# Kernel optimization log

Measured on AMD Instinct MI355X. Metric: run time of the kernel, lower is better.

## Reference

```python
import jax, jax.numpy as jnp
import numpy as np

B, S, D, H = 2, 2048, 1024, 16
RANK = int(D * 0.2)  # 204, per decom(): rank = int(min(a,b)*ratio_LR)
HEAD = D // H


def setup_inputs() -> dict:
    key = jax.random.key(0)
    ks = jax.random.split(key, 16)
    s_in = 1.0 / np.sqrt(D)
    s_r = 1.0 / np.sqrt(RANK)
    inp = {
        'q': jax.random.normal(ks[0], (B, S, D), jnp.float32),
        'k': jax.random.normal(ks[1], (B, S, D), jnp.float32),
        'v': jax.random.normal(ks[2], (B, S, D), jnp.float32),
    }
    names = ['q', 'k', 'v', 'o']
    for i, n in enumerate(names):
        inp[f'V{n}'] = jax.random.uniform(ks[3 + 3 * i], (RANK, D), jnp.float32, -s_in, s_in)
        inp[f'U{n}'] = jax.random.uniform(ks[4 + 3 * i], (D, RANK), jnp.float32, -s_r, s_r)
        inp[f'b{n}'] = jax.random.uniform(ks[5 + 3 * i], (D,), jnp.float32, -s_r, s_r)
    return inp


def _factorized(x, Vw, Uw, b):
    # x @ V^T @ U^T + b  (low-rank linear: Linear(D->rank, no bias) then Linear(rank->D, bias))
    return jnp.einsum('bsr,dr->bsd', jnp.einsum('bsd,rd->bsr', x, Vw), Uw) + b


def _split_heads(x):
    # [B,S,D] -> [B,H,S,HEAD]
    return x.reshape(B, S, H, HEAD).transpose(0, 2, 1, 3)


def reference(q, k, v, Vq, Uq, bq, Vk, Uk, bk, Vv, Uv, bv, Vo, Uo, bo):
    qh = _split_heads(_factorized(q, Vq, Uq, bq))
    kh = _split_heads(_factorized(k, Vk, Uk, bk))
    vh = _split_heads(_factorized(v, Vv, Uv, bv))
    temperature = jnp.asarray(HEAD, jnp.float32) ** 0.5
    scores = jnp.einsum('bhqd,bhkd->bhqk', qh, kh) / temperature
    causal = jnp.tril(jnp.ones((S, S), bool))  # recreated each call in original
    scores = jnp.where(causal, scores, -jnp.inf)
    attn = jax.nn.softmax(scores, axis=-1)  # [B,H,S,S]
    out = jnp.einsum('bhqk,bhkd->bhqd', attn, vh)
    out = out.transpose(0, 2, 1, 3).reshape(B, S, D)
    out = _factorized(out, Vo, Uo, bo)
    # original returns attn flattened over batch*heads
    return out, attn.reshape(B * H, S, S)
```

## Files before the change

### kernel.cpp

```cpp
#include <hip/hip_runtime.h>
#include <stdint.h>

#define BB   2
#define SS   2048
#define DD   1024
#define NH   16
#define RK   204
#define RKP  256
#define HDIM 64
#define BH   (BB*NH)

typedef __attribute__((ext_vector_type(8))) short short8;
typedef __attribute__((ext_vector_type(4))) float f32x4;
typedef unsigned short u16;
typedef unsigned int   u32;

#define NEGBIG (-1e30f)

static __device__ __forceinline__ u16 f2bf(float f) {
    union { float f; u32 u; } v; v.f = f;
    u32 u = v.u;
    return (u16)((u + 0x7fffu + ((u >> 16) & 1u)) >> 16);
}
static __device__ __forceinline__ u32 pack2(float lo, float hi) {
    return (u32)f2bf(lo) | ((u32)f2bf(hi) << 16);
}

__global__ void cvt_bf16_k(const float* __restrict__ in, u16* __restrict__ out, int n4) {
    int i = blockIdx.x * blockDim.x + threadIdx.x;
    if (i < n4) {
        float4 f = ((const float4*)in)[i];
        u32 lo = pack2(f.x, f.y), hi = pack2(f.z, f.w);
        ((uint2*)out)[i] = make_uint2(lo, hi);
    }
}

__global__ void cvt_pad_u_k(const float* __restrict__ in, u16* __restrict__ out) {
    int i = blockIdx.x * blockDim.x + threadIdx.x;
    if (i >= DD * RKP) return;
    int row = i >> 8, col = i & (RKP - 1);
    out[i] = (col < RK) ? f2bf(in[row * RK + col]) : (u16)0;
}

__global__ __launch_bounds__(256)
void transpose_v_k(const u16* __restrict__ vh, u16* __restrict__ vT) {
    __shared__ __align__(16) u16 T[64*72];
    const int blk = blockIdx.x;
    const int st = blk & 31, bh = blk >> 5;
    const int b_ = bh >> 4, h = bh & (NH - 1);
    const int t = threadIdx.x;
    const int r = t >> 2, seg = t & 3;

    const u16* src = vh + (size_t)(b_*SS + st*64 + r)*DD + h*HDIM + seg*16;
    __align__(16) u16 vs_[16];
    *(uint4*)(vs_ + 0) = ((const uint4*)src)[0];
    *(uint4*)(vs_ + 8) = ((const uint4*)src)[1];
    #pragma unroll
    for (int j = 0; j < 16; ++j) T[(seg*16 + j)*72 + r] = vs_[j];
    __syncthreads();

    u16* dst = vT + ((size_t)bh*HDIM + r)*SS + st*64 + seg*16;
    ((uint4*)dst)[0] = *(const uint4*)(T + r*72 + seg*16);
    ((uint4*)dst)[1] = *(const uint4*)(T + r*72 + seg*16 + 8);
}

template<int A_F32, int OUT_F32, int HAS_BIAS>
__global__ __launch_bounds__(256)
void gemm_nt_k(const void* __restrict__ Ap, int lda,
               const u16* __restrict__ Bp, int ldb, int nrowsB,
               const float* __restrict__ bias,
               void* __restrict__ Cp, int ldc, int K)
{
    __shared__ __align__(16) u16 As[64*72];
    __shared__ __align__(16) u16 Bs[64*72];
    const int row0 = blockIdx.x * 64;
    const int col0 = blockIdx.y * 64;
    const int t = threadIdx.x;
    const int w = t >> 6, lane = t & 63, quad = lane >> 4, l16 = lane & 15;
    const int r = t >> 2, seg = t & 3;

    f32x4 acc0 = 0.f, acc1 = 0.f, acc2 = 0.f, acc3 = 0.f;

    for (int k0 = 0; k0 < K; k0 += 64) {
        __syncthreads();
        if (A_F32) {
            const float* ga = (const float*)Ap + (size_t)(row0 + r) * lda + k0 + seg*16;
            float4 f0 = ((const float4*)ga)[0];
            float4 f1 = ((const float4*)ga)[1];
            float4 f2 = ((const float4*)ga)[2];
            float4 f3 = ((const float4*)ga)[3];
            uint4 s0 = { pack2(f0.x,f0.y), pack2(f0.z,f0.w), pack2(f1.x,f1.y), pack2(f1.z,f1.w) };
            uint4 s1 = { pack2(f2.x,f2.y), pack2(f2.z,f2.w), pack2(f3.x,f3.y), pack2(f3.z,f3.w) };
            *(uint4*)(As + r*72 + seg*16)     = s0;
            *(uint4*)(As + r*72 + seg*16 + 8) = s1;
        } else {
            const u16* ga = (const u16*)Ap + (size_t)(row0 + r) * lda + k0 + seg*16;
            *(uint4*)(As + r*72 + seg*16)     = ((const uint4*)ga)[0];
            *(uint4*)(As + r*72 + seg*16 + 8) = ((const uint4*)ga)[1];
        }
        {
            uint4 b0 = {0,0,0,0}, b1 = {0,0,0,0};
            if (col0 + r < nrowsB) {
                const u16* gb = Bp + (size_t)(col0 + r) * ldb + k0 + seg*16;
                b0 = ((const uint4*)gb)[0];
                b1 = ((const uint4*)gb)[1];
            }
            *(uint4*)(Bs + r*72 + seg*16)     = b0;
            *(uint4*)(Bs + r*72 + seg*16 + 8) = b1;
        }
        __syncthreads();
        #pragma unroll
        for (int c = 0; c < 2; ++c) {
            short8 a = *(const short8*)(As + (w*16 + l16)*72 + c*32 + quad*8);
            short8 b0v = *(const short8*)(Bs + (0*16 + l16)*72 + c*32 + quad*8);
            acc0 = __builtin_amdgcn_mfma_f32_16x16x32_bf16(a, b0v, acc0, 0, 0, 0);
            short8 b1v = *(const short8*)(Bs + (1*16 + l16)*72 + c*32 + quad*8);
            acc1 = __builtin_amdgcn_mfma_f32_16x16x32_bf16(a, b1v, acc1, 0, 0, 0);
            short8 b2v = *(const short8*)(Bs + (2*16 + l16)*72 + c*32 + quad*8);
            acc2 = __builtin_amdgcn_mfma_f32_16x16x32_bf16(a, b2v, acc2, 0, 0, 0);
            short8 b3v = *(const short8*)(Bs + (3*16 + l16)*72 + c*32 + quad*8);
            acc3 = __builtin_amdgcn_mfma_f32_16x16x32_bf16(a, b3v, acc3, 0, 0, 0);
        }
    }

    #pragma unroll
    for (int f = 0; f < 4; ++f) {
        f32x4 a = (f==0) ? acc0 : (f==1) ? acc1 : (f==2) ? acc2 : acc3;
        int col = col0 + f*16 + l16;
        float bv = HAS_BIAS ? bias[col] : 0.f;
        #pragma unroll
        for (int rg = 0; rg < 4; ++rg) {
            int rowg = row0 + w*16 + quad*4 + rg;
            float val = a[rg] + bv;
            if (col >= nrowsB) val = 0.f;
            if (OUT_F32) ((float*)Cp)[(size_t)rowg*ldc + col] = val;
            else         ((u16*)Cp)[(size_t)rowg*ldc + col]  = f2bf(val);
        }
    }
}

__global__ __launch_bounds__(256)
void attn_ml_k(const u16* __restrict__ qh, const u16* __restrict__ kh,
               float* __restrict__ mbuf, float* __restrict__ lbuf)
{
    __shared__ __align__(16) u16 Ks[64*72];
    const int blk = blockIdx.x;
    const int qt = blk & 31, bh = blk >> 5;
    const int b_ = bh >> 4, h = bh & (NH - 1);
    const int qbase = qt * 64;
    const int t = threadIdx.x, w = t >> 6, lane = t & 63, quad = lane >> 4, l16 = lane & 15;
    const int r = t >> 2, seg = t & 3;
    const float scl = 0.125f;

    const u16* qrow = qh + (size_t)(b_*SS + qbase + w*16 + l16)*DD + h*HDIM;
    short8 q0 = *(const short8*)(qrow + quad*8);
    short8 q1 = *(const short8*)(qrow + 32 + quad*8);

    float m[4], l[4];
    #pragma unroll
    for (int rg = 0; rg < 4; ++rg) { m[rg] = NEGBIG; l[rg] = 0.f; }

    for (int kt = 0; kt <= qt; ++kt) {
        int kbase = kt * 64;
        __syncthreads();
        const u16* krow = kh + (size_t)(b_*SS + kbase + r)*DD + h*HDIM + seg*16;
        uint4 kv0 = ((const uint4*)krow)[0];
        uint4 kv1 = ((const uint4*)krow)[1];
        *(uint4*)(Ks + r*72 + seg*16)     = kv0;
        *(uint4*)(Ks + r*72 + seg*16 + 8) = kv1;
        __syncthreads();

        f32x4 sa0 = 0.f, sa1 = 0.f, sa2 = 0.f, sa3 = 0.f;
        {
            short8 b0 = *(const short8*)(Ks + (0*16 + l16)*72 + quad*8);
            sa0 = __builtin_amdgcn_mfma_f32_16x16x32_bf16(q0, b0, sa0, 0,0,0);
            short8 b0b = *(const short8*)(Ks + (0*16 + l16)*72 + 32 + quad*8);
            sa0 = __builtin_amdgcn_mfma_f32_16x16x32_bf16(q1, b0b, sa0, 0,0,0);
            short8 b1 = *(const short8*)(Ks + (1*16 + l16)*72 + quad*8);
            sa1 = __builtin_amdgcn_mfma_f32_16x16x32_bf16(q0, b1, sa1, 0,0,0);
            short8 b1b = *(const short8*)(Ks + (1*16 + l16)*72 + 32 + quad*8);
            sa1 = __builtin_amdgcn_mfma_f32_16x16x32_bf16(q1, b1b, sa1, 0,0,0);
            short8 b2 = *(const short8*)(Ks + (2*16 + l16)*72 + quad*8);
            sa2 = __builtin_amdgcn_mfma_f32_16x16x32_bf16(q0, b2, sa2, 0,0,0);
            short8 b2b = *(const short8*)(Ks + (2*16 + l16)*72 + 32 + quad*8);
            sa2 = __builtin_amdgcn_mfma_f32_16x16x32_bf16(q1, b2b, sa2, 0,0,0);
            short8 b3 = *(const short8*)(Ks + (3*16 + l16)*72 + quad*8);
            sa3 = __builtin_amdgcn_mfma_f32_16x16x32_bf16(q0, b3, sa3, 0,0,0);
            short8 b3b = *(const short8*)(Ks + (3*16 + l16)*72 + 32 + quad*8);
            sa3 = __builtin_amdgcn_mfma_f32_16x16x32_bf16(q1, b3b, sa3, 0,0,0);
        }

        if (kt < qt) {
            #pragma unroll
            for (int rg = 0; rg < 4; ++rg) {
                float v0 = sa0[rg]*scl, v1 = sa1[rg]*scl, v2 = sa2[rg]*scl, v3 = sa3[rg]*scl;
                float m4 = fmaxf(fmaxf(v0, v1), fmaxf(v2, v3));
                float nm = fmaxf(m[rg], m4);
                l[rg] = l[rg]*__expf(m[rg]-nm)
                      + (__expf(v0-nm)+__expf(v1-nm)) + (__expf(v2-nm)+__expf(v3-nm));
                m[rg] = nm;
            }
        } else {
            int key0 = kbase + l16;
            #pragma unroll
            for (int rg = 0; rg < 4; ++rg) {
                int qg = qbase + w*16 + quad*4 + rg;
                bool c0 = (key0      <= qg), c1 = (key0 + 16 <= qg);
                bool c2 = (key0 + 32 <= qg), c3 = (key0 + 48 <= qg);
                float v0 = c0 ? sa0[rg]*scl : NEGBIG;
                float v1 = c1 ? sa1[rg]*scl : NEGBIG;
                float v2 = c2 ? sa2[rg]*scl : NEGBIG;
                float v3 = c3 ? sa3[rg]*scl : NEGBIG;
                float m4 = fmaxf(fmaxf(v0, v1), fmaxf(v2, v3));
                float nm = fmaxf(m[rg], m4);
                float e0 = c0 ? __expf(v0-nm) : 0.f;
                float e1 = c1 ? __expf(v1-nm) : 0.f;
                float e2 = c2 ? __expf(v2-nm) : 0.f;
                float e3 = c3 ? __expf(v3-nm) : 0.f;
                float corr = (m[rg] > NEGBIG) ? __expf(m[rg]-nm) : 0.f;
                l[rg] = l[rg]*corr + (e0+e1) + (e2+e3);
                m[rg] = nm;
            }
        }
    }

    #pragma unroll
    for (int rg = 0; rg < 4; ++rg) {
        #pragma unroll
        for (int d = 1; d < 16; d <<= 1) {
            float mo = __shfl_xor(m[rg], d);
            float lo = __shfl_xor(l[rg], d);
            float nm = fmaxf(m[rg], mo);
            l[rg] = l[rg]*__expf(m[rg]-nm) + lo*__expf(mo-nm);
            m[rg] = nm;
        }
    }
    if (l16 == 0) {
        #pragma unroll
        for (int rg = 0; rg < 4; ++rg) {
            int qg = qbase + w*16 + quad*4 + rg;
            mbuf[bh*SS + qg] = m[rg];
            lbuf[bh*SS + qg] = l[rg];
        }
    }
}

__global__ __launch_bounds__(256)
void attn_av_k(const u16* __restrict__ qh, const u16* __restrict__ kh,
               const u16* __restrict__ vT,
               const float* __restrict__ mbuf, const float* __restrict__ lbuf,
               float* __restrict__ attn_out, u16* __restrict__ Ob)
{
    __shared__ __align__(16) u16 Ks[64*72];
    __shared__ __align__(16) u16 Vs[64*72];
    __shared__ __align__(16) u16 Ps[64*72];
    const int blk = blockIdx.x;
    const int qt = blk & 31, bh = blk >> 5;
    const int b_ = bh >> 4, h = bh & (NH - 1);
    const int qbase = qt * 64;
    const int t = threadIdx.x, w = t >> 6, lane = t & 63, quad = lane >> 4, l16 = lane & 15;
    const int r = t >> 2, seg = t & 3;
    const float scl = 0.125f;

    const u16* qrow = qh + (size_t)(b_*SS + qbase + w*16 + l16)*DD + h*HDIM;
    short8 q0 = *(const short8*)(qrow + quad*8);
    short8 q1 = *(const short8*)(qrow + 32 + quad*8);

    float mr[4], rl[4];
    #pragma unroll
    for (int rg = 0; rg < 4; ++rg) {
        int qg = qbase + w*16 + quad*4 + rg;
        mr[rg] = mbuf[bh*SS + qg];
        rl[rg] = 1.f / lbuf[bh*SS + qg];
    }
    f32x4 oa0 = 0.f, oa1 = 0.f, oa2 = 0.f, oa3 = 0.f;
    float* attn_base = attn_out + (size_t)bh * SS * SS;

    for (int kt = 0; kt <= qt; ++kt) {
        int kbase = kt * 64;
        __syncthreads();
        {
            const u16* krow = kh + (size_t)(b_*SS + kbase + r)*DD + h*HDIM + seg*16;
            *(uint4*)(Ks + r*72 + seg*16)     = ((const uint4*)krow)[0];
            *(uint4*)(Ks + r*72 + seg*16 + 8) = ((const uint4*)krow)[1];
            const u16* vrow = vT + ((size_t)(bh*HDIM + r))*SS + kbase + seg*16;
            *(uint4*)(Vs + r*72 + seg*16)     = ((const uint4*)vrow)[0];
            *(uint4*)(Vs + r*72 + seg*16 + 8) = ((const uint4*)vrow)[1];
        }
        __syncthreads();

        f32x4 sa0 = 0.f, sa1 = 0.f, sa2 = 0.f, sa3 = 0.f;
        {
            short8 b0 = *(const short8*)(Ks + (0*16 + l16)*72 + quad*8);
            sa0 = __builtin_amdgcn_mfma_f32_16x16x32_bf16(q0, b0, sa0, 0,0,0);
            short8 b0b = *(const short8*)(Ks + (0*16 + l16)*72 + 32 + quad*8);
            sa0 = __builtin_amdgcn_mfma_f32_16x16x32_bf16(q1, b0b, sa0, 0,0,0);
            short8 b1 = *(const short8*)(Ks + (1*16 + l16)*72 + quad*8);
            sa1 = __builtin_amdgcn_mfma_f32_16x16x32_bf16(q0, b1, sa1, 0,0,0);
            short8 b1b = *(const short8*)(Ks + (1*16 + l16)*72 + 32 + quad*8);
            sa1 = __builtin_amdgcn_mfma_f32_16x16x32_bf16(q1, b1b, sa1, 0,0,0);
            short8 b2 = *(const short8*)(Ks + (2*16 + l16)*72 + quad*8);
            sa2 = __builtin_amdgcn_mfma_f32_16x16x32_bf16(q0, b2, sa2, 0,0,0);
            short8 b2b = *(const short8*)(Ks + (2*16 + l16)*72 + 32 + quad*8);
            sa2 = __builtin_amdgcn_mfma_f32_16x16x32_bf16(q1, b2b, sa2, 0,0,0);
            short8 b3 = *(const short8*)(Ks + (3*16 + l16)*72 + quad*8);
            sa3 = __builtin_amdgcn_mfma_f32_16x16x32_bf16(q0, b3, sa3, 0,0,0);
            short8 b3b = *(const short8*)(Ks + (3*16 + l16)*72 + 32 + quad*8);
            sa3 = __builtin_amdgcn_mfma_f32_16x16x32_bf16(q1, b3b, sa3, 0,0,0);
        }

        if (kt < qt) {
            #pragma unroll
            for (int f = 0; f < 4; ++f) {
                f32x4 sv = (f==0) ? sa0 : (f==1) ? sa1 : (f==2) ? sa2 : sa3;
                int key = kbase + f*16 + l16;
                #pragma unroll
                for (int rg = 0; rg < 4; ++rg) {
                    int qg = qbase + w*16 + quad*4 + rg;
                    float p = __expf(sv[rg]*scl - mr[rg]) * rl[rg];
                    attn_base[(size_t)qg*SS + key] = p;
                    Ps[(w*16 + quad*4 + rg)*72 + f*16 + l16] = f2bf(p);
                }
            }
        } else {
            #pragma unroll
            for (int f = 0; f < 4; ++f) {
                f32x4 sv = (f==0) ? sa0 : (f==1) ? sa1 : (f==2) ? sa2 : sa3;
                int key = kbase + f*16 + l16;
                #pragma unroll
                for (int rg = 0; rg < 4; ++rg) {
                    int qg = qbase + w*16 + quad*4 + rg;
                    float p = (key <= qg) ? __expf(sv[rg]*scl - mr[rg]) * rl[rg] : 0.f;
                    attn_base[(size_t)qg*SS + key] = p;
                    Ps[(w*16 + quad*4 + rg)*72 + f*16 + l16] = f2bf(p);
                }
            }
        }
        asm volatile("" ::: "memory");

        #pragma unroll
        for (int c = 0; c < 2; ++c) {
            short8 pa = *(const short8*)(Ps + (w*16 + l16)*72 + c*32 + quad*8);
            short8 v0 = *(const short8*)(Vs + (0*16 + l16)*72 + c*32 + quad*8);
            oa0 = __builtin_amdgcn_mfma_f32_16x16x32_bf16(pa, v0, oa0, 0,0,0);
            short8 v1 = *(const short8*)(Vs + (1*16 + l16)*72 + c*32 + quad*8);
            oa1 = __builtin_amdgcn_mfma_f32_16x16x32_bf16(pa, v1, oa1, 0,0,0);
            short8 v2 = *(const short8*)(Vs + (2*16 + l16)*72 + c*32 + quad*8);
            oa2 = __builtin_amdgcn_mfma_f32_16x16x32_bf16(pa, v2, oa2, 0,0,0);
            short8 v3 = *(const short8*)(Vs + (3*16 + l16)*72 + c*32 + quad*8);
            oa3 = __builtin_amdgcn_mfma_f32_16x16x32_bf16(pa, v3, oa3, 0,0,0);
        }
    }

    for (int kt = qt + 1; kt < 32; ++kt) {
        int kbase = kt * 64;
        float4 z = {0.f, 0.f, 0.f, 0.f};
        float* p = attn_base + (size_t)(qbase + r)*SS + kbase + seg*16;
        ((float4*)p)[0] = z; ((float4*)p)[1] = z; ((float4*)p)[2] = z; ((float4*)p)[3] = z;
    }

    #pragma unroll
    for (int f = 0; f < 4; ++f) {
        f32x4 ov = (f==0) ? oa0 : (f==1) ? oa1 : (f==2) ? oa2 : oa3;
        #pragma unroll
        for (int rg = 0; rg < 4; ++rg) {
            int qg = qbase + w*16 + quad*4 + rg;
            Ob[(size_t)(b_*SS + qg)*DD + h*HDIM + f*16 + l16] = f2bf(ov[rg]);
        }
    }
}

extern "C" void kernel_launch(void* const* d_in, const int* in_sizes, int n_in,
                              void* d_out, int out_size, void* d_ws, size_t ws_size,
                              hipStream_t stream)
{
    const float* xs[3] = { (const float*)d_in[0], (const float*)d_in[1], (const float*)d_in[2] };
    const float* Vw[4] = { (const float*)d_in[3], (const float*)d_in[6], (const float*)d_in[9],  (const float*)d_in[12] };
    const float* Uw[4] = { (const float*)d_in[4], (const float*)d_in[7], (const float*)d_in[10], (const float*)d_in[13] };
    const float* bw[4] = { (const float*)d_in[5], (const float*)d_in[8], (const float*)d_in[11], (const float*)d_in[14] };

    char* ws = (char*)d_ws;
    size_t off = 0;
    auto alloc = [&](size_t bytes) -> char* {
        char* p = ws + off;
        off += (bytes + 255) & ~(size_t)255;
        return p;
    };
    u16* wV[4]; for (int i = 0; i < 4; ++i) wV[i] = (u16*)alloc((size_t)RK*DD*2);
    u16* wU[4]; for (int i = 0; i < 4; ++i) wU[i] = (u16*)alloc((size_t)DD*RKP*2);
    u16* Tb  = (u16*)alloc((size_t)BB*SS*RKP*2);
    u16* hb[3]; for (int i = 0; i < 3; ++i) hb[i] = (u16*)alloc((size_t)BB*SS*DD*2);
    u16* vTb = (u16*)alloc((size_t)BB*SS*DD*2);
    float* mbuf = (float*)alloc((size_t)BH*SS*4);
    float* lbuf = (float*)alloc((size_t)BH*SS*4);
    u16* Ob  = (u16*)alloc((size_t)BB*SS*DD*2);
    (void)ws_size; (void)in_sizes; (void)n_in; (void)out_size;

    for (int i = 0; i < 4; ++i)
        cvt_bf16_k<<<(RK*DD/4 + 255)/256, 256, 0, stream>>>(Vw[i], wV[i], RK*DD/4);
    for (int i = 0; i < 4; ++i)
        cvt_pad_u_k<<<(DD*RKP + 255)/256, 256, 0, stream>>>(Uw[i], wU[i]);

    const int MROWS = BB*SS;
    for (int p = 0; p < 3; ++p) {
        gemm_nt_k<1,0,0><<<dim3(MROWS/64, RKP/64), 256, 0, stream>>>(
            xs[p], DD, wV[p], DD, RK, nullptr, Tb, RKP, DD);
        gemm_nt_k<0,0,1><<<dim3(MROWS/64, DD/64), 256, 0, stream>>>(
            Tb, RKP, wU[p], RKP, DD, bw[p], hb[p], DD, RKP);
    }
    transpose_v_k<<<BH*32, 256, 0, stream>>>(hb[2], vTb);

    float* attn_out = (float*)d_out + (size_t)BB*SS*DD;
    attn_ml_k<<<BH*32, 256, 0, stream>>>(hb[0], hb[1], mbuf, lbuf);
    attn_av_k<<<BH*32, 256, 0, stream>>>(hb[0], hb[1], vTb, mbuf, lbuf, attn_out, Ob);

    gemm_nt_k<0,0,0><<<dim3(MROWS/64, RKP/64), 256, 0, stream>>>(
        Ob, DD, wV[3], DD, RK, nullptr, Tb, RKP, DD);
    gemm_nt_k<0,1,1><<<dim3(MROWS/64, DD/64), 256, 0, stream>>>(
        Tb, RKP, wU[3], RKP, DD, bw[3], d_out, DD, RKP);
}
```

Baseline: 837.1 us.

## Fuse attention passes, V transpose into GEMM epilogue, nontemporal attn stores

Merges the two attention kernels (row max/sum pass and probability/AV pass) into one kernel that runs both passes back-to-back per query tile. This keeps m/l in registers instead of a global buffer round trip and saves a launch. The V projection GEMM now writes its output already transposed through shared memory, which removes the separate transpose kernel and one full intermediate buffer. Stores of the large fp32 attention matrix become nontemporal to cut cache pollution. The fused kernel holds more shared memory and registers per block, which may reduce occupancy.

```diff
diff --git a/kernel.cpp b/kernel.cpp
--- a/kernel.cpp
+++ b/kernel.cpp
@@ -42,29 +42,7 @@
     out[i] = (col < RK) ? f2bf(in[row * RK + col]) : (u16)0;
 }
 
-__global__ __launch_bounds__(256)
-void transpose_v_k(const u16* __restrict__ vh, u16* __restrict__ vT) {
-    __shared__ __align__(16) u16 T[64*72];
-    const int blk = blockIdx.x;
-    const int st = blk & 31, bh = blk >> 5;
-    const int b_ = bh >> 4, h = bh & (NH - 1);
-    const int t = threadIdx.x;
-    const int r = t >> 2, seg = t & 3;
-
-    const u16* src = vh + (size_t)(b_*SS + st*64 + r)*DD + h*HDIM + seg*16;
-    __align__(16) u16 vs_[16];
-    *(uint4*)(vs_ + 0) = ((const uint4*)src)[0];
-    *(uint4*)(vs_ + 8) = ((const uint4*)src)[1];
-    #pragma unroll
-    for (int j = 0; j < 16; ++j) T[(seg*16 + j)*72 + r] = vs_[j];
-    __syncthreads();
-
-    u16* dst = vT + ((size_t)bh*HDIM + r)*SS + st*64 + seg*16;
-    ((uint4*)dst)[0] = *(const uint4*)(T + r*72 + seg*16);
-    ((uint4*)dst)[1] = *(const uint4*)(T + r*72 + seg*16 + 8);
-}
-
-template<int A_F32, int OUT_F32, int HAS_BIAS>
+template<int A_F32, int OUT_F32, int HAS_BIAS, int OUT_VT>
 __global__ __launch_bounds__(256)
 void gemm_nt_k(const void* __restrict__ Ap, int lda,
                const u16* __restrict__ Bp, int ldb, int nrowsB,
@@ -123,6 +101,29 @@
         }
     }
 
+    if (OUT_VT) {
+        __syncthreads();
+        #pragma unroll
+        for (int f = 0; f < 4; ++f) {
+            f32x4 a = (f==0) ? acc0 : (f==1) ? acc1 : (f==2) ? acc2 : acc3;
+            int col = f*16 + l16;
+            float bv = HAS_BIAS ? bias[col0 + col] : 0.f;
+            #pragma unroll
+            for (int rg = 0; rg < 4; ++rg) {
+                int rowl = w*16 + quad*4 + rg;
+                As[col*72 + rowl] = f2bf(a[rg] + bv);
+            }
+        }
+        __syncthreads();
+        const int b_ = row0 >> 11;
+        const int s0 = row0 & (SS - 1);
+        const int h  = col0 >> 6;
+        u16* dst = (u16*)Cp + ((size_t)((b_*NH + h)*HDIM + r))*SS + s0 + seg*16;
+        ((uint4*)dst)[0] = *(const uint4*)(As + r*72 + seg*16);
+        ((uint4*)dst)[1] = *(const uint4*)(As + r*72 + seg*16 + 8);
+        return;
+    }
+
     #pragma unroll
     for (int f = 0; f < 4; ++f) {
         f32x4 a = (f==0) ? acc0 : (f==1) ? acc1 : (f==2) ? acc2 : acc3;
@@ -139,11 +140,33 @@
     }
 }
 
+#define QKT_8(sa0,sa1,sa2,sa3) do { \
+    short8 b0 = *(const short8*)(Ks + (0*16 + l16)*72 + quad*8); \
+    sa0 = __builtin_amdgcn_mfma_f32_16x16x32_bf16(q0, b0, sa0, 0,0,0); \
+    short8 b0b = *(const short8*)(Ks + (0*16 + l16)*72 + 32 + quad*8); \
+    sa0 = __builtin_amdgcn_mfma_f32_16x16x32_bf16(q1, b0b, sa0, 0,0,0); \
+    short8 b1 = *(const short8*)(Ks + (1*16 + l16)*72 + quad*8); \
+    sa1 = __builtin_amdgcn_mfma_f32_16x16x32_bf16(q0, b1, sa1, 0,0,0); \
+    short8 b1b = *(const short8*)(Ks + (1*16 + l16)*72 + 32 + quad*8); \
+    sa1 = __builtin_amdgcn_mfma_f32_16x16x32_bf16(q1, b1b, sa1, 0,0,0); \
+    short8 b2 = *(const short8*)(Ks + (2*16 + l16)*72 + quad*8); \
+    sa2 = __builtin_amdgcn_mfma_f32_16x16x32_bf16(q0, b2, sa2, 0,0,0); \
+    short8 b2b = *(const short8*)(Ks + (2*16 + l16)*72 + 32 + quad*8); \
+    sa2 = __builtin_amdgcn_mfma_f32_16x16x32_bf16(q1, b2b, sa2, 0,0,0); \
+    short8 b3 = *(const short8*)(Ks + (3*16 + l16)*72 + quad*8); \
+    sa3 = __builtin_amdgcn_mfma_f32_16x16x32_bf16(q0, b3, sa3, 0,0,0); \
+    short8 b3b = *(const short8*)(Ks + (3*16 + l16)*72 + 32 + quad*8); \
+    sa3 = __builtin_amdgcn_mfma_f32_16x16x32_bf16(q1, b3b, sa3, 0,0,0); \
+} while (0)
+
 __global__ __launch_bounds__(256)
-void attn_ml_k(const u16* __restrict__ qh, const u16* __restrict__ kh,
-               float* __restrict__ mbuf, float* __restrict__ lbuf)
+void attn_k(const u16* __restrict__ qh, const u16* __restrict__ kh,
+            const u16* __restrict__ vT,
+            float* __restrict__ attn_out, u16* __restrict__ Ob)
 {
     __shared__ __align__(16) u16 Ks[64*72];
+    __shared__ __align__(16) u16 Vs[64*72];
+    __shared__ __align__(16) u16 Ps[64*72];
     const int blk = blockIdx.x;
     const int qt = blk & 31, bh = blk >> 5;
     const int b_ = bh >> 4, h = bh & (NH - 1);
@@ -156,39 +179,24 @@
     short8 q0 = *(const short8*)(qrow + quad*8);
     short8 q1 = *(const short8*)(qrow + 32 + quad*8);
 
+    const u16* kstage = kh + (size_t)(b_*SS + r)*DD + h*HDIM + seg*16;
+    const u16* vstage = vT + ((size_t)(bh*HDIM + r))*SS + seg*16;
+
     float m[4], l[4];
     #pragma unroll
     for (int rg = 0; rg < 4; ++rg) { m[rg] = NEGBIG; l[rg] = 0.f; }
 
     for (int kt = 0; kt <= qt; ++kt) {
-        int kbase = kt * 64;
-        __syncthreads();
-        const u16* krow = kh + (size_t)(b_*SS + kbase + r)*DD + h*HDIM + seg*16;
-        uint4 kv0 = ((const uint4*)krow)[0];
-        uint4 kv1 = ((const uint4*)krow)[1];
-        *(uint4*)(Ks + r*72 + seg*16)     = kv0;
-        *(uint4*)(Ks + r*72 + seg*16 + 8) = kv1;
+        __syncthreads();
+        {
+            const u16* krow = kstage + (size_t)kt*64*DD;
+            *(uint4*)(Ks + r*72 + seg*16)     = ((const uint4*)krow)[0];
+            *(uint4*)(Ks + r*72 + seg*16 + 8) = ((const uint4*)krow)[1];
+        }
         __syncthreads();
 
         f32x4 sa0 = 0.f, sa1 = 0.f, sa2 = 0.f, sa3 = 0.f;
-        {
-            short8 b0 = *(const short8*)(Ks + (0*16 + l16)*72 + quad*8);
-            sa0 = __builtin_amdgcn_mfma_f32_16x16x32_bf16(q0, b0, sa0, 0,0,0);
-            short8 b0b = *(const short8*)(Ks + (0*16 + l16)*72 + 32 + quad*8);
-            sa0 = __builtin_amdgcn_mfma_f32_16x16x32_bf16(q1, b0b, sa0, 0,0,0);
-            short8 b1 = *(const short8*)(Ks + (1*16 + l16)*72 + quad*8);
-            sa1 = __builtin_amdgcn_mfma_f32_16x16x32_bf16(q0, b1, sa1, 0,0,0);
-            short8 b1b = *(const short8*)(Ks + (1*16 + l16)*72 + 32 + quad*8);
-            sa1 = __builtin_amdgcn_mfma_f32_16x16x32_bf16(q1, b1b, sa1, 0,0,0);
-            short8 b2 = *(const short8*)(Ks + (2*16 + l16)*72 + quad*8);
-            sa2 = __builtin_amdgcn_mfma_f32_16x16x32_bf16(q0, b2, sa2, 0,0,0);
-            short8 b2b = *(const short8*)(Ks + (2*16 + l16)*72 + 32 + quad*8);
-            sa2 = __builtin_amdgcn_mfma_f32_16x16x32_bf16(q1, b2b, sa2, 0,0,0);
-            short8 b3 = *(const short8*)(Ks + (3*16 + l16)*72 + quad*8);
-            sa3 = __builtin_amdgcn_mfma_f32_16x16x32_bf16(q0, b3, sa3, 0,0,0);
-            short8 b3b = *(const short8*)(Ks + (3*16 + l16)*72 + 32 + quad*8);
-            sa3 = __builtin_amdgcn_mfma_f32_16x16x32_bf16(q1, b3b, sa3, 0,0,0);
-        }
+        QKT_8(sa0, sa1, sa2, sa3);
 
         if (kt < qt) {
             #pragma unroll
@@ -201,7 +209,7 @@
                 m[rg] = nm;
             }
         } else {
-            int key0 = kbase + l16;
+            int key0 = kt*64 + l16;
             #pragma unroll
             for (int rg = 0; rg < 4; ++rg) {
                 int qg = qbase + w*16 + quad*4 + rg;
@@ -235,94 +243,51 @@
             m[rg] = nm;
         }
     }
-    if (l16 == 0) {
-        #pragma unroll
-        for (int rg = 0; rg < 4; ++rg) {
-            int qg = qbase + w*16 + quad*4 + rg;
-            mbuf[bh*SS + qg] = m[rg];
-            lbuf[bh*SS + qg] = l[rg];
-        }
-    }
-}
-
-__global__ __launch_bounds__(256)
-void attn_av_k(const u16* __restrict__ qh, const u16* __restrict__ kh,
-               const u16* __restrict__ vT,
-               const float* __restrict__ mbuf, const float* __restrict__ lbuf,
-               float* __restrict__ attn_out, u16* __restrict__ Ob)
-{
-    __shared__ __align__(16) u16 Ks[64*72];
-    __shared__ __align__(16) u16 Vs[64*72];
-    __shared__ __align__(16) u16 Ps[64*72];
-    const int blk = blockIdx.x;
-    const int qt = blk & 31, bh = blk >> 5;
-    const int b_ = bh >> 4, h = bh & (NH - 1);
-    const int qbase = qt * 64;
-    const int t = threadIdx.x, w = t >> 6, lane = t & 63, quad = lane >> 4, l16 = lane & 15;
-    const int r = t >> 2, seg = t & 3;
-    const float scl = 0.125f;
-
-    const u16* qrow = qh + (size_t)(b_*SS + qbase + w*16 + l16)*DD + h*HDIM;
-    short8 q0 = *(const short8*)(qrow + quad*8);
-    short8 q1 = *(const short8*)(qrow + 32 + quad*8);
-
     float mr[4], rl[4];
     #pragma unroll
-    for (int rg = 0; rg < 4; ++rg) {
-        int qg = qbase + w*16 + quad*4 + rg;
-        mr[rg] = mbuf[bh*SS + qg];
-        rl[rg] = 1.f / lbuf[bh*SS + qg];
-    }
+    for (int rg = 0; rg < 4; ++rg) { mr[rg] = m[rg]; rl[rg] = 1.f / l[rg]; }
+
     f32x4 oa0 = 0.f, oa1 = 0.f, oa2 = 0.f, oa3 = 0.f;
     float* attn_base = attn_out + (size_t)bh * SS * SS;
+    float* rp0 = attn_base + (size_t)(qbase + w*16 + quad*4 + 0)*SS + l16;
+    float* rp1 = attn_base + (size_t)(qbase + w*16 + quad*4 + 1)*SS + l16;
+    float* rp2 = attn_base + (size_t)(qbase + w*16 + quad*4 + 2)*SS + l16;
+    float* rp3 = attn_base + (size_t)(qbase + w*16 + quad*4 + 3)*SS + l16;
 
     for (int kt = 0; kt <= qt; ++kt) {
-        int kbase = kt * 64;
         __syncthreads();
         {
-            const u16* krow = kh + (size_t)(b_*SS + kbase + r)*DD + h*HDIM + seg*16;
+            const u16* krow = kstage + (size_t)kt*64*DD;
             *(uint4*)(Ks + r*72 + seg*16)     = ((const uint4*)krow)[0];
             *(uint4*)(Ks + r*72 + seg*16 + 8) = ((const uint4*)krow)[1];
-            const u16* vrow = vT + ((size_t)(bh*HDIM + r))*SS + kbase + seg*16;
+            const u16* vrow = vstage + kt*64;
             *(uint4*)(Vs + r*72 + seg*16)     = ((const uint4*)vrow)[0];
             *(uint4*)(Vs + r*72 + seg*16 + 8) = ((const uint4*)vrow)[1];
         }
         __syncthreads();
 
         f32x4 sa0 = 0.f, sa1 = 0.f, sa2 = 0.f, sa3 = 0.f;
-        {
-            short8 b0 = *(const short8*)(Ks + (0*16 + l16)*72 + quad*8);
-            sa0 = __builtin_amdgcn_mfma_f32_16x16x32_bf16(q0, b0, sa0, 0,0,0);
-            short8 b0b = *(const short8*)(Ks + (0*16 + l16)*72 + 32 + quad*8);
-            sa0 = __builtin_amdgcn_mfma_f32_16x16x32_bf16(q1, b0b, sa0, 0,0,0);
-            short8 b1 = *(const short8*)(Ks + (1*16 + l16)*72 + quad*8);
-            sa1 = __builtin_amdgcn_mfma_f32_16x16x32_bf16(q0, b1, sa1, 0,0,0);
-            short8 b1b = *(const short8*)(Ks + (1*16 + l16)*72 + 32 + quad*8);
-            sa1 = __builtin_amdgcn_mfma_f32_16x16x32_bf16(q1, b1b, sa1, 0,0,0);
-            short8 b2 = *(const short8*)(Ks + (2*16 + l16)*72 + quad*8);
-            sa2 = __builtin_amdgcn_mfma_f32_16x16x32_bf16(q0, b2, sa2, 0,0,0);
-            short8 b2b = *(const short8*)(Ks + (2*16 + l16)*72 + 32 + quad*8);
-            sa2 = __builtin_amdgcn_mfma_f32_16x16x32_bf16(q1, b2b, sa2, 0,0,0);
-            short8 b3 = *(const short8*)(Ks + (3*16 + l16)*72 + quad*8);
-            sa3 = __builtin_amdgcn_mfma_f32_16x16x32_bf16(q0, b3, sa3, 0,0,0);
-            short8 b3b = *(const short8*)(Ks + (3*16 + l16)*72 + 32 + quad*8);
-            sa3 = __builtin_amdgcn_mfma_f32_16x16x32_bf16(q1, b3b, sa3, 0,0,0);
-        }
+        QKT_8(sa0, sa1, sa2, sa3);
 
         if (kt < qt) {
             #pragma unroll
             for (int f = 0; f < 4; ++f) {
                 f32x4 sv = (f==0) ? sa0 : (f==1) ? sa1 : (f==2) ? sa2 : sa3;
-                int key = kbase + f*16 + l16;
-                #pragma unroll
-                for (int rg = 0; rg < 4; ++rg) {
-                    int qg = qbase + w*16 + quad*4 + rg;
-                    float p = __expf(sv[rg]*scl - mr[rg]) * rl[rg];
-                    attn_base[(size_t)qg*SS + key] = p;
-                    Ps[(w*16 + quad*4 + rg)*72 + f*16 + l16] = f2bf(p);
-                }
+                float p0 = __expf(sv[0]*scl - mr[0]) * rl[0];
+                float p1 = __expf(sv[1]*scl - mr[1]) * rl[1];
+                float p2 = __expf(sv[2]*scl - mr[2]) * rl[2];
+                float p3 = __expf(sv[3]*scl - mr[3]) * rl[3];
+                __builtin_nontemporal_store(p0, rp0 + f*16);
+                __builtin_nontemporal_store(p1, rp1 + f*16);
+                __builtin_nontemporal_store(p2, rp2 + f*16);
+                __builtin_nontemporal_store(p3, rp3 + f*16);
+                Ps[(w*16 + quad*4 + 0)*72 + f*16 + l16] = f2bf(p0);
+                Ps[(w*16 + quad*4 + 1)*72 + f*16 + l16] = f2bf(p1);
+                Ps[(w*16 + quad*4 + 2)*72 + f*16 + l16] = f2bf(p2);
+                Ps[(w*16 + quad*4 + 3)*72 + f*16 + l16] = f2bf(p3);
             }
         } else {
+            int kbase = kt*64;
             #pragma unroll
             for (int f = 0; f < 4; ++f) {
                 f32x4 sv = (f==0) ? sa0 : (f==1) ? sa1 : (f==2) ? sa2 : sa3;
@@ -331,11 +296,14 @@
                 for (int rg = 0; rg < 4; ++rg) {
                     int qg = qbase + w*16 + quad*4 + rg;
                     float p = (key <= qg) ? __expf(sv[rg]*scl - mr[rg]) * rl[rg] : 0.f;
-                    attn_base[(size_t)qg*SS + key] = p;
+                    float* rp = (rg==0) ? rp0 : (rg==1) ? rp1 : (rg==2) ? rp2 : rp3;
+                    __builtin_nontemporal_store(p, rp + f*16);
                     Ps[(w*16 + quad*4 + rg)*72 + f*16 + l16] = f2bf(p);
                 }
             }
         }
+        rp0 += 64; rp1 += 64; rp2 += 64; rp3 += 64;
+
         asm volatile("" ::: "memory");
 
         #pragma unroll
@@ -354,9 +322,12 @@
 
     for (int kt = qt + 1; kt < 32; ++kt) {
         int kbase = kt * 64;
-        float4 z = {0.f, 0.f, 0.f, 0.f};
+        f32x4 z = 0.f;
         float* p = attn_base + (size_t)(qbase + r)*SS + kbase + seg*16;
-        ((float4*)p)[0] = z; ((float4*)p)[1] = z; ((float4*)p)[2] = z; ((float4*)p)[3] = z;
+        __builtin_nontemporal_store(z, (f32x4*)p + 0);
+        __builtin_nontemporal_store(z, (f32x4*)p + 1);
+        __builtin_nontemporal_store(z, (f32x4*)p + 2);
+        __builtin_nontemporal_store(z, (f32x4*)p + 3);
     }
 
     #pragma unroll
@@ -389,10 +360,8 @@
     u16* wV[4]; for (int i = 0; i < 4; ++i) wV[i] = (u16*)alloc((size_t)RK*DD*2);
     u16* wU[4]; for (int i = 0; i < 4; ++i) wU[i] = (u16*)alloc((size_t)DD*RKP*2);
     u16* Tb  = (u16*)alloc((size_t)BB*SS*RKP*2);
-    u16* hb[3]; for (int i = 0; i < 3; ++i) hb[i] = (u16*)alloc((size_t)BB*SS*DD*2);
+    u16* hb[2]; for (int i = 0; i < 2; ++i) hb[i] = (u16*)alloc((size_t)BB*SS*DD*2);
     u16* vTb = (u16*)alloc((size_t)BB*SS*DD*2);
-    float* mbuf = (float*)alloc((size_t)BH*SS*4);
-    float* lbuf = (float*)alloc((size_t)BH*SS*4);
     u16* Ob  = (u16*)alloc((size_t)BB*SS*DD*2);
     (void)ws_size; (void)in_sizes; (void)n_in; (void)out_size;
 
@@ -402,20 +371,22 @@
         cvt_pad_u_k<<<(DD*RKP + 255)/256, 256, 0, stream>>>(Uw[i], wU[i]);
 
     const int MROWS = BB*SS;
-    for (int p = 0; p < 3; ++p) {
-        gemm_nt_k<1,0,0><<<dim3(MROWS/64, RKP/64), 256, 0, stream>>>(
+    for (int p = 0; p < 2; ++p) {
+        gemm_nt_k<1,0,0,0><<<dim3(MROWS/64, RKP/64), 256, 0, stream>>>(
             xs[p], DD, wV[p], DD, RK, nullptr, Tb, RKP, DD);
-        gemm_nt_k<0,0,1><<<dim3(MROWS/64, DD/64), 256, 0, stream>>>(
+        gemm_nt_k<0,0,1,0><<<dim3(MROWS/64, DD/64), 256, 0, stream>>>(
             Tb, RKP, wU[p], RKP, DD, bw[p], hb[p], DD, RKP);
     }
-    transpose_v_k<<<BH*32, 256, 0, stream>>>(hb[2], vTb);
+    gemm_nt_k<1,0,0,0><<<dim3(MROWS/64, RKP/64), 256, 0, stream>>>(
+        xs[2], DD, wV[2], DD, RK, nullptr, Tb, RKP, DD);
+    gemm_nt_k<0,0,1,1><<<dim3(MROWS/64, DD/64), 256, 0, stream>>>(
+        Tb, RKP, wU[2], RKP, DD, bw[2], vTb, DD, RKP);
 
     float* attn_out = (float*)d_out + (size_t)BB*SS*DD;
-    attn_ml_k<<<BH*32, 256, 0, stream>>>(hb[0], hb[1], mbuf, lbuf);
-    attn_av_k<<<BH*32, 256, 0, stream>>>(hb[0], hb[1], vTb, mbuf, lbuf, attn_out, Ob);
-
-    gemm_nt_k<0,0,0><<<dim3(MROWS/64, RKP/64), 256, 0, stream>>>(
+    attn_k<<<BH*32, 256, 0, stream>>>(hb[0], hb[1], vTb, attn_out, Ob);
+
+    gemm_nt_k<0,0,0,0><<<dim3(MROWS/64, RKP/64), 256, 0, stream>>>(
         Ob, DD, wV[3], DD, RK, nullptr, Tb, RKP, DD);
-    gemm_nt_k<0,1,1><<<dim3(MROWS/64, DD/64), 256, 0, stream>>>(
+    gemm_nt_k<0,1,1,0><<<dim3(MROWS/64, DD/64), 256, 0, stream>>>(
         Tb, RKP, wU[3], RKP, DD, bw[3], d_out, DD, RKP);
 }
```

After: 1.169 ms. 1.4x slower.
